# Kernel optimization log

Hardware: AMD Instinct MI355X
Metric: run time of the kernel (lower is better)

## Reference

```python
import jax, jax.numpy as jnp
import numpy as np

B, N, E, P = 8, 4096, 16384, 64   # batch, num_nodes, num_edges, query poses per scene
D, H, MSG, UPD = 256, 512, 256, 254  # node_dim, MLP hidden, msg_sz, update_sz


def setup_inputs() -> dict:
    key = jax.random.key(0)
    ks = jax.random.split(key, 12)
    s = 0.02  # weight scale
    inp = {
        'nodes_states': jax.random.normal(ks[0], (B, N, D), jnp.float32),
        'attn': jax.random.uniform(ks[1], (B, P, N), jnp.float32),
        'W_e1': (jax.random.normal(ks[2], (2 * D, H), jnp.float32) * s),
        'b_e1': jnp.zeros((H,), jnp.float32),
        'W_e2': (jax.random.normal(ks[3], (H, MSG), jnp.float32) * s),
        'b_e2': jnp.zeros((MSG,), jnp.float32),
        'W_n1': (jax.random.normal(ks[4], (D + MSG, H), jnp.float32) * s),
        'b_n1': jnp.zeros((H,), jnp.float32),
        'W_n2': (jax.random.normal(ks[5], (H, UPD), jnp.float32) * s),
        'b_n2': jnp.zeros((UPD,), jnp.float32),
        'edge_sources': jax.random.randint(ks[6], (E,), 0, N, jnp.int32),
        'edge_sinks': jax.random.randint(ks[7], (E,), 0, N, jnp.int32),
        'msg_steps': 3,
    }
    return inp


def reference(nodes_states, attn, W_e1, b_e1, W_e2, b_e2, W_n1, b_n1, W_n2, b_n2,
              edge_sources, edge_sinks, msg_steps):
    ns = nodes_states  # (B, N, D)
    upd_sz = W_n2.shape[-1]
    for _ in range(int(msg_steps)):
        # gather node states along edges
        src = ns[:, edge_sources]            # (B, E, D)
        snk = ns[:, edge_sinks]              # (B, E, D)
        e_in = jnp.concatenate([src, snk], axis=-1)          # (B, E, 2D)
        h = jax.nn.relu(e_in @ W_e1 + b_e1)
        msgs = h @ W_e2 + b_e2                               # (B, E, MSG)
        # scatter-add messages to sink nodes (== torch index_add on dim 1)
        incoming = jnp.zeros((ns.shape[0], ns.shape[1], msgs.shape[-1]), ns.dtype)
        incoming = incoming.at[:, edge_sinks].add(msgs)      # (B, N, MSG)
        # node update MLP
        n_in = jnp.concatenate([incoming, ns], axis=-1)      # (B, N, D+MSG)
        h2 = jax.nn.relu(n_in @ W_n1 + b_n1)
        upd = h2 @ W_n2 + b_n2                               # (B, N, UPD)
        ns = ns.at[:, :, -upd_sz:].add(upd)
    # graph_out_to_out: attention-weighted extraction (torch.bmm)
    extraction = jnp.einsum('bpn,bnd->bpd', attn, ns)        # (B, P, D)
    # num_copies = 0 -> extraction unchanged; unsqueeze(-1).unsqueeze(-1)
    return extraction[..., None, None]
```

## Files before the change

### kernel.cpp

```cpp
#include <hip/hip_runtime.h>
#include <cstddef>
#include <cstdint>

typedef unsigned short u16;
typedef unsigned int u32;
typedef short bf16x8 __attribute__((ext_vector_type(8)));
typedef float f32x4 __attribute__((ext_vector_type(4)));
typedef u32 u32x4 __attribute__((ext_vector_type(4)));

namespace {
constexpr int B_ = 8, N_ = 4096, E_ = 16384, P_ = 64;
constexpr int D_ = 256, H_ = 512, MSG_ = 256, UPD_ = 254;
constexpr int CHUNK_U16 = 16384;
constexpr int NCHUNK = 24;
constexpr float FXS = 16384.0f;
constexpr float FXI = 1.0f / 16384.0f;
}

__device__ inline u16 f2b(float f) {
  u32 u = __float_as_uint(f);
  u += 0x7FFFu + ((u >> 16) & 1u);
  return (u16)(u >> 16);
}
__device__ inline u32 pk2(float a, float b) {
  return (u32)f2b(a) | ((u32)f2b(b) << 16);
}
__device__ inline f32x4 mfma16(bf16x8 a, bf16x8 b, f32x4 c) {
  return __builtin_amdgcn_mfma_f32_16x16x32_bf16(a, b, c, 0, 0, 0);
}
__device__ inline void gload16(const void* g, void* l) {
  __builtin_amdgcn_global_load_lds(
      (const __attribute__((address_space(1))) unsigned int*)g,
      (__attribute__((address_space(3))) unsigned int*)l, 16, 0, 0);
}
__device__ inline void wait_vm8()   { asm volatile("s_waitcnt vmcnt(8)" ::: "memory"); }
__device__ inline void wait_vm0()   { asm volatile("s_waitcnt vmcnt(0)" ::: "memory"); }
__device__ inline void wait_lgkm0() { asm volatile("s_waitcnt lgkmcnt(0)" ::: "memory"); }

__global__ void hist_k(const int* __restrict__ esnk, int* __restrict__ cnt) {
  const int e = blockIdx.x * 256 + threadIdx.x;
  atomicAdd(&cnt[esnk[e]], 1);
}
__global__ __launch_bounds__(256)
void scan_k(const int* __restrict__ cnt, int* __restrict__ rowptr,
            int* __restrict__ cursor) {
  __shared__ int part[257];
  const int t = threadIdx.x;
  int c[16]; int s = 0;
#pragma unroll
  for (int i = 0; i < 16; i++) { c[i] = cnt[t * 16 + i]; s += c[i]; }
  part[t + 1] = s;
  __syncthreads();
  if (t == 0) { part[0] = 0; for (int i = 1; i <= 256; i++) part[i] += part[i - 1]; }
  __syncthreads();
  int off = part[t];
#pragma unroll
  for (int i = 0; i < 16; i++) {
    rowptr[t * 16 + i] = off; cursor[t * 16 + i] = off; off += c[i];
  }
}
__global__ void place_k(const int* __restrict__ esnk, int* __restrict__ cursor,
                        int* __restrict__ order) {
  const int e = blockIdx.x * 256 + threadIdx.x;
  const int p = atomicAdd(&cursor[esnk[e]], 1);
  order[p] = e;
}

__global__ void b16cast_k(const float* __restrict__ src, u16* __restrict__ dst) {
  const int i = blockIdx.x * 256 + threadIdx.x;
  const float4 v0 = ((const float4*)src)[i * 2];
  const float4 v1 = ((const float4*)src)[i * 2 + 1];
  u32x4 pk;
  pk.x = pk2(v0.x, v0.y); pk.y = pk2(v0.z, v0.w);
  pk.z = pk2(v1.x, v1.y); pk.w = pk2(v1.z, v1.w);
  ((u32x4*)dst)[i] = pk;
}

__global__ __launch_bounds__(256, 2)
void edge_mlp(const u16* __restrict__ nsb, u16* __restrict__ msgs,
              const int* __restrict__ esrc, const int* __restrict__ esnk,
              const u16* __restrict__ wpk,
              const float* __restrict__ b1, const float* __restrict__ b2, int g0)
{
  __shared__ alignas(16) u16 Wbuf[2 * CHUNK_U16];

  const int t = threadIdx.x;
  const int w = t >> 6, l = t & 63, r = l & 15, lq = l >> 4;
  const int bl = blockIdx.y, bb = g0 + bl;
  const int e0 = blockIdx.x * 128 + w * 32 + r;
  const int e1 = e0 + 16;

  auto stage = [&](int c, int buf) {
    const u16* gb = wpk + (size_t)c * CHUNK_U16;
    u16* lb = &Wbuf[buf * CHUNK_U16];
#pragma unroll
    for (int s = 0; s < 8; s++) {
      const int sidx = s * 256 + t;
      gload16(gb + (size_t)sidx * 8, lb + sidx * 8);
    }
  };
  stage(0, 0);

  const int nrs0 = esrc[e0], nrk0 = esnk[e0];
  const int nrs1 = esrc[e1], nrk1 = esnk[e1];

  bf16x8 af[2][16];
#pragma unroll
  for (int kt = 0; kt < 16; kt++) {
    const int co = (kt < 8 ? kt : kt - 8) * 32 + lq * 8;
    const int n0 = (kt < 8) ? nrs0 : nrk0;
    const int n1 = (kt < 8) ? nrs1 : nrk1;
    af[0][kt] = *(const bf16x8*)(nsb + ((size_t)bb * N_ + n0) * 256 + co);
    af[1][kt] = *(const bf16x8*)(nsb + ((size_t)bb * N_ + n1) * 256 + co);
  }

  const int s0 = ((2 * lq) & 3) * 16 + r;
  const int s1 = ((2 * lq + 1) & 3) * 16 + r;
  const bool sel = (lq >> 1) != 0;

  auto mk_hB = [&](f32x4 a0, f32x4 a1, float4 bv0, float4 bv1) -> bf16x8 {
    const u32 p00 = pk2(fmaxf(a0[0] + bv0.x, 0.f), fmaxf(a0[1] + bv0.y, 0.f));
    const u32 p01 = pk2(fmaxf(a0[2] + bv0.z, 0.f), fmaxf(a0[3] + bv0.w, 0.f));
    const u32 p10 = pk2(fmaxf(a1[0] + bv1.x, 0.f), fmaxf(a1[1] + bv1.y, 0.f));
    const u32 p11 = pk2(fmaxf(a1[2] + bv1.z, 0.f), fmaxf(a1[3] + bv1.w, 0.f));
    const int t00 = __shfl((int)p00, s0), t10 = __shfl((int)p10, s0);
    const int t01 = __shfl((int)p01, s0), t11 = __shfl((int)p11, s0);
    const int u00 = __shfl((int)p00, s1), u10 = __shfl((int)p10, s1);
    const int u01 = __shfl((int)p01, s1), u11 = __shfl((int)p11, s1);
    u32x4 hb;
    hb.x = (u32)(sel ? t10 : t00); hb.y = (u32)(sel ? t11 : t01);
    hb.z = (u32)(sel ? u10 : u00); hb.w = (u32)(sel ? u11 : u01);
    return __builtin_bit_cast(bf16x8, hb);
  };

  bf16x8 hB[2][16];

#pragma unroll
  for (int P = 0; P < 16; P++) {
    wait_lgkm0();
    __builtin_amdgcn_s_barrier();
    stage(P + 1, (P + 1) & 1);
    wait_vm8();
    __builtin_amdgcn_s_barrier();
    __builtin_amdgcn_sched_barrier(0);
    f32x4 a00 = {}, a01 = {}, a10 = {}, a11 = {};
    const u16* wb = &Wbuf[(P & 1) * CHUNK_U16];
    __builtin_amdgcn_s_setprio(1);
#pragma unroll
    for (int kt = 0; kt < 16; kt++) {
      const bf16x8 w0 = *(const bf16x8*)&wb[((kt * 2 + 0) * 64 + l) * 8];
      const bf16x8 w1 = *(const bf16x8*)&wb[((kt * 2 + 1) * 64 + l) * 8];
      a00 = mfma16(w0, af[0][kt], a00);
      a01 = mfma16(w1, af[0][kt], a01);
      a10 = mfma16(w0, af[1][kt], a10);
      a11 = mfma16(w1, af[1][kt], a11);
    }
    __builtin_amdgcn_s_setprio(0);
    const float4 bv0 = *(const float4*)(b1 + P * 32 + lq * 4);
    const float4 bv1 = *(const float4*)(b1 + P * 32 + 16 + lq * 4);
    hB[0][P] = mk_hB(a00, a01, bv0, bv1);
    hB[1][P] = mk_hB(a10, a11, bv0, bv1);
  }

  u16* mrow0 = msgs + ((size_t)bl * E_ + e0) * 256;
  u16* mrow1 = msgs + ((size_t)bl * E_ + e1) * 256;
#pragma unroll
  for (int Hh = 0; Hh < 2; Hh++) {
    f32x4 acc[4][2][2] = {};
#pragma unroll
    for (int cc = 0; cc < 4; cc++) {
      const int C = Hh * 4 + cc, c = 16 + C;
      wait_lgkm0();
      __builtin_amdgcn_s_barrier();
      if (C < 7) { stage(c + 1, (c + 1) & 1); wait_vm8(); }
      else       { wait_vm0(); }
      __builtin_amdgcn_s_barrier();
      __builtin_amdgcn_sched_barrier(0);
      const u16* wb = &Wbuf[(c & 1) * CHUNK_U16];
      __builtin_amdgcn_s_setprio(1);
#pragma unroll
      for (int kt = 0; kt < 16; kt++) {
        const bf16x8 w0 = *(const bf16x8*)&wb[((kt * 2 + 0) * 64 + l) * 8];
        const bf16x8 w1 = *(const bf16x8*)&wb[((kt * 2 + 1) * 64 + l) * 8];
        acc[cc][0][0] = mfma16(w0, hB[0][kt], acc[cc][0][0]);
        acc[cc][0][1] = mfma16(w1, hB[0][kt], acc[cc][0][1]);
        acc[cc][1][0] = mfma16(w0, hB[1][kt], acc[cc][1][0]);
        acc[cc][1][1] = mfma16(w1, hB[1][kt], acc[cc][1][1]);
      }
      __builtin_amdgcn_s_setprio(0);
    }
#pragma unroll
    for (int cc = 0; cc < 4; cc++) {
      const int C = Hh * 4 + cc;
      const float4 bv0 = *(const float4*)(b2 + C * 32 + lq * 4);
      const float4 bv1 = *(const float4*)(b2 + C * 32 + 16 + lq * 4);
      uint2 q0, q1;
      q0.x = pk2(acc[cc][0][0][0] + bv0.x, acc[cc][0][0][1] + bv0.y);
      q0.y = pk2(acc[cc][0][0][2] + bv0.z, acc[cc][0][0][3] + bv0.w);
      q1.x = pk2(acc[cc][0][1][0] + bv1.x, acc[cc][0][1][1] + bv1.y);
      q1.y = pk2(acc[cc][0][1][2] + bv1.z, acc[cc][0][1][3] + bv1.w);
      *(uint2*)&mrow0[C * 32 + lq * 4]      = q0;
      *(uint2*)&mrow0[C * 32 + 16 + lq * 4] = q1;
      uint2 r0, r1;
      r0.x = pk2(acc[cc][1][0][0] + bv0.x, acc[cc][1][0][1] + bv0.y);
      r0.y = pk2(acc[cc][1][0][2] + bv0.z, acc[cc][1][0][3] + bv0.w);
      r1.x = pk2(acc[cc][1][1][0] + bv1.x, acc[cc][1][1][1] + bv1.y);
      r1.y = pk2(acc[cc][1][1][2] + bv1.z, acc[cc][1][1][3] + bv1.w);
      *(uint2*)&mrow1[C * 32 + lq * 4]      = r0;
      *(uint2*)&mrow1[C * 32 + 16 + lq * 4] = r1;
    }
  }
}

__global__ __launch_bounds__(256)
void gather_k(const u16* __restrict__ msgs, u16* __restrict__ incb,
              const int* __restrict__ order, const int* __restrict__ rowptr,
              const int* __restrict__ cnt, int g0)
{
  const int t = threadIdx.x;
  const int n = blockIdx.x * 4 + (t >> 6);
  const int l = t & 63;
  const int bl = blockIdx.y, bb = g0 + bl;
  const int c0 = l * 4;
  int sA = 0, sB = 0, sC = 0, sD = 0;
  const int beg = rowptr[n], num = cnt[n];
  for (int i = 0; i < num; i++) {
    const int e = order[beg + i];
    const uint2 p = *(const uint2*)(msgs + ((size_t)bl * E_ + e) * 256 + c0);
    sA += __float2int_rn(__uint_as_float(p.x << 16) * FXS);
    sB += __float2int_rn(__uint_as_float(p.x & 0xFFFF0000u) * FXS);
    sC += __float2int_rn(__uint_as_float(p.y << 16) * FXS);
    sD += __float2int_rn(__uint_as_float(p.y & 0xFFFF0000u) * FXS);
  }
  uint2 o;
  o.x = pk2((float)sA * FXI, (float)sB * FXI);
  o.y = pk2((float)sC * FXI, (float)sD * FXI);
  *(uint2*)(incb + ((size_t)bb * N_ + n) * 256 + c0) = o;
}

__global__ __launch_bounds__(256, 1)
void node_mlp(float* __restrict__ ns, u16* __restrict__ nsb,
              const u16* __restrict__ incb, const u16* __restrict__ wpk,
              const float* __restrict__ b1, const float* __restrict__ b2)
{
  __shared__ alignas(16) u16 Wbuf[2 * CHUNK_U16];

  const int t = threadIdx.x;
  const int w = t >> 6, l = t & 63, r = l & 15, lq = l >> 4;
  const int bb = blockIdx.y;
  const int row0 = blockIdx.x * 128 + w * 32 + r;
  const int row1 = row0 + 16;

  auto stage = [&](int c, int buf) {
    const u16* gb = wpk + (size_t)c * CHUNK_U16;
    u16* lb = &Wbuf[buf * CHUNK_U16];
#pragma unroll
    for (int s = 0; s < 8; s++) {
      const int sidx = s * 256 + t;
      gload16(gb + (size_t)sidx * 8, lb + sidx * 8);
    }
  };
  stage(0, 0);

  bf16x8 af[2][16];
#pragma unroll
  for (int kt = 0; kt < 16; kt++) {
    if (kt < 8) {
      af[0][kt] = *(const bf16x8*)(incb + ((size_t)bb * N_ + row0) * 256 + kt * 32 + lq * 8);
      af[1][kt] = *(const bf16x8*)(incb + ((size_t)bb * N_ + row1) * 256 + kt * 32 + lq * 8);
    } else {
      const int co = (kt - 8) * 32 + lq * 8;
      af[0][kt] = *(const bf16x8*)(nsb + ((size_t)bb * N_ + row0) * 256 + co);
      af[1][kt] = *(const bf16x8*)(nsb + ((size_t)bb * N_ + row1) * 256 + co);
    }
  }

  const int s0 = ((2 * lq) & 3) * 16 + r;
  const int s1 = ((2 * lq + 1) & 3) * 16 + r;
  const bool sel = (lq >> 1) != 0;

  auto mk_hB = [&](f32x4 a0, f32x4 a1, float4 bv0, float4 bv1) -> bf16x8 {
    const u32 p00 = pk2(fmaxf(a0[0] + bv0.x, 0.f), fmaxf(a0[1] + bv0.y, 0.f));
    const u32 p01 = pk2(fmaxf(a0[2] + bv0.z, 0.f), fmaxf(a0[3] + bv0.w, 0.f));
    const u32 p10 = pk2(fmaxf(a1[0] + bv1.x, 0.f), fmaxf(a1[1] + bv1.y, 0.f));
    const u32 p11 = pk2(fmaxf(a1[2] + bv1.z, 0.f), fmaxf(a1[3] + bv1.w, 0.f));
    const int t00 = __shfl((int)p00, s0), t10 = __shfl((int)p10, s0);
    const int t01 = __shfl((int)p01, s0), t11 = __shfl((int)p11, s0);
    const int u00 = __shfl((int)p00, s1), u10 = __shfl((int)p10, s1);
    const int u01 = __shfl((int)p01, s1), u11 = __shfl((int)p11, s1);
    u32x4 hb;
    hb.x = (u32)(sel ? t10 : t00); hb.y = (u32)(sel ? t11 : t01);
    hb.z = (u32)(sel ? u10 : u00); hb.w = (u32)(sel ? u11 : u01);
    return __builtin_bit_cast(bf16x8, hb);
  };

  bf16x8 hB[2][16];

#pragma unroll
  for (int P = 0; P < 16; P++) {
    wait_lgkm0();
    __builtin_amdgcn_s_barrier();
    stage(P + 1, (P + 1) & 1);
    wait_vm8();
    __builtin_amdgcn_s_barrier();
    __builtin_amdgcn_sched_barrier(0);
    f32x4 a00 = {}, a01 = {}, a10 = {}, a11 = {};
    const u16* wb = &Wbuf[(P & 1) * CHUNK_U16];
    __builtin_amdgcn_s_setprio(1);
#pragma unroll
    for (int kt = 0; kt < 16; kt++) {
      const bf16x8 w0 = *(const bf16x8*)&wb[((kt * 2 + 0) * 64 + l) * 8];
      const bf16x8 w1 = *(const bf16x8*)&wb[((kt * 2 + 1) * 64 + l) * 8];
      a00 = mfma16(w0, af[0][kt], a00);
      a01 = mfma16(w1, af[0][kt], a01);
      a10 = mfma16(w0, af[1][kt], a10);
      a11 = mfma16(w1, af[1][kt], a11);
    }
    __builtin_amdgcn_s_setprio(0);
    const float4 bv0 = *(const float4*)(b1 + P * 32 + lq * 4);
    const float4 bv1 = *(const float4*)(b1 + P * 32 + 16 + lq * 4);
    hB[0][P] = mk_hB(a00, a01, bv0, bv1);
    hB[1][P] = mk_hB(a10, a11, bv0, bv1);
  }

  float* nsrow0 = ns + ((size_t)bb * N_ + row0) * 256;
  float* nsrow1 = ns + ((size_t)bb * N_ + row1) * 256;
  u16* mbrow0 = nsb + ((size_t)bb * N_ + row0) * 256;
  u16* mbrow1 = nsb + ((size_t)bb * N_ + row1) * 256;
#pragma unroll
  for (int Hh = 0; Hh < 2; Hh++) {
    f32x4 acc[4][2][2] = {};
#pragma unroll
    for (int cc = 0; cc < 4; cc++) {
      const int C = Hh * 4 + cc, c = 16 + C;
      wait_lgkm0();
      __builtin_amdgcn_s_barrier();
      if (C < 7) { stage(c + 1, (c + 1) & 1); wait_vm8(); }
      else       { wait_vm0(); }
      __builtin_amdgcn_s_barrier();
      __builtin_amdgcn_sched_barrier(0);
      const u16* wb = &Wbuf[(c & 1) * CHUNK_U16];
      __builtin_amdgcn_s_setprio(1);
#pragma unroll
      for (int kt = 0; kt < 16; kt++) {
        const bf16x8 w0 = *(const bf16x8*)&wb[((kt * 2 + 0) * 64 + l) * 8];
        const bf16x8 w1 = *(const bf16x8*)&wb[((kt * 2 + 1) * 64 + l) * 8];
        acc[cc][0][0] = mfma16(w0, hB[0][kt], acc[cc][0][0]);
        acc[cc][0][1] = mfma16(w1, hB[0][kt], acc[cc][0][1]);
        acc[cc][1][0] = mfma16(w0, hB[1][kt], acc[cc][1][0]);
        acc[cc][1][1] = mfma16(w1, hB[1][kt], acc[cc][1][1]);
      }
      __builtin_amdgcn_s_setprio(0);
    }
#pragma unroll
    for (int cc = 0; cc < 4; cc++) {
      const int C = Hh * 4 + cc;
      const float4 bv0 = *(const float4*)(b2 + C * 32 + lq * 4);
      const float4 bv1 = *(const float4*)(b2 + C * 32 + 16 + lq * 4);
      const int uA = C * 32 + lq * 4, uB = uA + 16;
#pragma unroll
      for (int g = 0; g < 2; g++) {
        float* nsrow = g ? nsrow1 : nsrow0;
        u16* mrow = g ? mbrow1 : mbrow0;
        const f32x4 a0 = acc[cc][g][0], a1 = acc[cc][g][1];
        float2* pA = (float2*)(nsrow + 2 + uA);
        float2 v0 = pA[0]; v0.x += a0[0] + bv0.x; v0.y += a0[1] + bv0.y; pA[0] = v0;
        float2 v1 = pA[1]; v1.x += a0[2] + bv0.z; v1.y += a0[3] + bv0.w; pA[1] = v1;
        *(u32*)(mrow + 2 + uA)     = pk2(v0.x, v0.y);
        *(u32*)(mrow + 2 + uA + 2) = pk2(v1.x, v1.y);
        float2* pB = (float2*)(nsrow + 2 + uB);
        float2 u0 = pB[0]; u0.x += a1[0] + bv1.x; u0.y += a1[1] + bv1.y; pB[0] = u0;
        *(u32*)(mrow + 2 + uB) = pk2(u0.x, u0.y);
        if (uB + 3 < UPD_) {
          float2 u1 = pB[1]; u1.x += a1[2] + bv1.z; u1.y += a1[3] + bv1.w; pB[1] = u1;
          *(u32*)(mrow + 2 + uB + 2) = pk2(u1.x, u1.y);
        }
      }
    }
  }
}

__global__ void pack_w(const float* __restrict__ W1, const float* __restrict__ W2,
                       int ldw2, int nv2, u16* __restrict__ out)
{
  const int idx = blockIdx.x * 256 + threadIdx.x;
  const int c = idx >> 11, s = idx & 2047;
  const int kt = s >> 7, i01 = (s >> 6) & 1, l = s & 63;
  const int r = l & 15, lq = l >> 4;
  const int kbase = kt * 32 + lq * 8;
  const int colt = i01 * 16 + r;
  u16 v[8];
  if (c < 16) {
    const int col = c * 32 + colt;
#pragma unroll
    for (int i = 0; i < 8; i++) v[i] = f2b(W1[(size_t)(kbase + i) * 512 + col]);
  } else {
    const int n2 = (c - 16) * 32 + colt;
#pragma unroll
    for (int i = 0; i < 8; i++)
      v[i] = (n2 < nv2) ? f2b(W2[(size_t)(kbase + i) * ldw2 + n2]) : (u16)0;
  }
  u32x4 pk;
  pk.x = (u32)v[0] | ((u32)v[1] << 16);
  pk.y = (u32)v[2] | ((u32)v[3] << 16);
  pk.z = (u32)v[4] | ((u32)v[5] << 16);
  pk.w = (u32)v[6] | ((u32)v[7] << 16);
  *(u32x4*)(out + (size_t)idx * 8) = pk;
}

__global__ __launch_bounds__(256)
void extract_k(const float* __restrict__ attn, const float* __restrict__ nsb,
               float* __restrict__ out)
{
  __shared__ float a_s[16][64];
  const int b = blockIdx.x, pc = blockIdx.y, kc = blockIdx.z;
  const int d = threadIdx.x;
  float acc[16] = {};
  const int nbase0 = kc * 128;

  for (int nb = 0; nb < 128; nb += 64) {
    const int nbase = nbase0 + nb;
    __syncthreads();
#pragma unroll
    for (int lp = 0; lp < 4; lp++) {
      const int idx = lp * 256 + threadIdx.x;
      const int pi = idx >> 6, j = idx & 63;
      a_s[pi][j] = attn[((size_t)b * P_ + pc * 16 + pi) * N_ + nbase + j];
    }
    __syncthreads();
#pragma unroll 8
    for (int j = 0; j < 64; j++) {
      const float v = nsb[((size_t)b * N_ + nbase + j) * D_ + d];
#pragma unroll
      for (int i = 0; i < 16; i++) acc[i] += a_s[i][j] * v;
    }
  }
#pragma unroll
  for (int i = 0; i < 16; i++)
    atomicAdd(&out[((size_t)b * P_ + pc * 16 + i) * D_ + d], acc[i]);
}

extern "C" void kernel_launch(void* const* d_in, const int* in_sizes, int n_in,
                              void* d_out, int out_size, void* d_ws, size_t ws_size,
                              hipStream_t stream)
{
  const float* nodes = (const float*)d_in[0];
  const float* attn  = (const float*)d_in[1];
  const float* W_e1  = (const float*)d_in[2];
  const float* b_e1  = (const float*)d_in[3];
  const float* W_e2  = (const float*)d_in[4];
  const float* b_e2  = (const float*)d_in[5];
  const float* W_n1  = (const float*)d_in[6];
  const float* b_n1  = (const float*)d_in[7];
  const float* W_n2  = (const float*)d_in[8];
  const float* b_n2  = (const float*)d_in[9];
  const int* esrc    = (const int*)d_in[10];
  const int* esnk    = (const int*)d_in[11];

  float* ns   = (float*)d_ws;
  u16* incb   = (u16*)(ns + (size_t)B_ * N_ * D_);
  u16* nsb16  = incb + (size_t)B_ * N_ * MSG_;
  u16* msgs   = nsb16 + (size_t)B_ * N_ * D_;

  const size_t fixed_b = (size_t)B_ * N_ * D_ * 4 + (size_t)B_ * N_ * MSG_ * 2
                       + (size_t)B_ * N_ * D_ * 2
                       + (size_t)2 * NCHUNK * CHUNK_U16 * 2 + (size_t)16 * N_ + 4096;
  const int gb = (ws_size >= fixed_b + (size_t)4 * E_ * MSG_ * 2) ? 4 : 2;

  u16* wpkE   = msgs + (size_t)gb * E_ * MSG_;
  u16* wpkN   = wpkE + (size_t)NCHUNK * CHUNK_U16;
  int* cnt    = (int*)(wpkN + (size_t)NCHUNK * CHUNK_U16);
  int* rowptr = cnt + N_;
  int* cursor = rowptr + N_;
  int* order  = cursor + N_;
  float* out  = (float*)d_out;

  hipMemcpyAsync(ns, nodes, sizeof(float) * (size_t)B_ * N_ * D_,
                 hipMemcpyDeviceToDevice, stream);
  b16cast_k<<<dim3(B_ * N_ * D_ / 8 / 256), dim3(256), 0, stream>>>(nodes, nsb16);
  pack_w<<<dim3(192), dim3(256), 0, stream>>>(W_e1, W_e2, MSG_, MSG_, wpkE);
  pack_w<<<dim3(192), dim3(256), 0, stream>>>(W_n1, W_n2, UPD_, UPD_, wpkN);

  hipMemsetAsync(cnt, 0, sizeof(int) * N_, stream);
  hist_k<<<dim3(E_ / 256), dim3(256), 0, stream>>>(esnk, cnt);
  scan_k<<<dim3(1), dim3(256), 0, stream>>>(cnt, rowptr, cursor);
  place_k<<<dim3(E_ / 256), dim3(256), 0, stream>>>(esnk, cursor, order);

  for (int s = 0; s < 3; s++) {
    for (int g0 = 0; g0 < B_; g0 += gb) {
      edge_mlp<<<dim3(E_ / 128, gb), dim3(256), 0, stream>>>(
          nsb16, msgs, esrc, esnk, wpkE, b_e1, b_e2, g0);
      gather_k<<<dim3(N_ / 4, gb), dim3(256), 0, stream>>>(
          msgs, incb, order, rowptr, cnt, g0);
    }
    node_mlp<<<dim3(N_ / 128, B_), dim3(256), 0, stream>>>(
        ns, nsb16, incb, wpkN, b_n1, b_n2);
  }

  hipMemsetAsync(out, 0, sizeof(float) * (size_t)out_size, stream);
  extract_k<<<dim3(B_, P_ / 16, 32), dim3(256), 0, stream>>>(attn, ns, out);
}
```

Baseline: 800.1 us.

## Interleave weight-chunk prefetch with MFMA loop and use single barrier per chunk

Weight chunk staging into LDS moves from a block of eight global-to-LDS loads before each chunk into the MFMA inner loop, one load per kt iteration. The two barriers and the vmcnt(8) wait per chunk become a single boundary after the chunk's compute that waits for all loads and LDS reads. The aim is to overlap the weight fetch with matrix work and cut barrier overhead, in both the edge and node MLP kernels. The trade-off is a full vmcnt(0) wait at every chunk, so any load latency not hidden by the compute is exposed directly.

```diff
diff --git a/kernel.cpp b/kernel.cpp
--- a/kernel.cpp
+++ b/kernel.cpp
@@ -33,9 +33,14 @@
       (const __attribute__((address_space(1))) unsigned int*)g,
       (__attribute__((address_space(3))) unsigned int*)l, 16, 0, 0);
 }
-__device__ inline void wait_vm8()   { asm volatile("s_waitcnt vmcnt(8)" ::: "memory"); }
 __device__ inline void wait_vm0()   { asm volatile("s_waitcnt vmcnt(0)" ::: "memory"); }
 __device__ inline void wait_lgkm0() { asm volatile("s_waitcnt lgkmcnt(0)" ::: "memory"); }
+__device__ inline void chunk_boundary() {
+  wait_lgkm0();
+  wait_vm0();
+  __builtin_amdgcn_s_barrier();
+  __builtin_amdgcn_sched_barrier(0);
+}
 
 __global__ void hist_k(const int* __restrict__ esnk, int* __restrict__ cnt) {
   const int e = blockIdx.x * 256 + threadIdx.x;
@@ -90,16 +95,14 @@
   const int e0 = blockIdx.x * 128 + w * 32 + r;
   const int e1 = e0 + 16;
 
-  auto stage = [&](int c, int buf) {
+  auto stage1 = [&](int c, int s) {
     const u16* gb = wpk + (size_t)c * CHUNK_U16;
-    u16* lb = &Wbuf[buf * CHUNK_U16];
-#pragma unroll
-    for (int s = 0; s < 8; s++) {
-      const int sidx = s * 256 + t;
-      gload16(gb + (size_t)sidx * 8, lb + sidx * 8);
-    }
+    u16* lb = &Wbuf[(c & 1) * CHUNK_U16];
+    const int sidx = s * 256 + t;
+    gload16(gb + (size_t)sidx * 8, lb + sidx * 8);
   };
-  stage(0, 0);
+#pragma unroll
+  for (int s = 0; s < 8; s++) stage1(0, s);
 
   const int nrs0 = esrc[e0], nrk0 = esnk[e0];
   const int nrs1 = esrc[e1], nrk1 = esnk[e1];
@@ -113,6 +116,7 @@
     af[0][kt] = *(const bf16x8*)(nsb + ((size_t)bb * N_ + n0) * 256 + co);
     af[1][kt] = *(const bf16x8*)(nsb + ((size_t)bb * N_ + n1) * 256 + co);
   }
+  chunk_boundary();
 
   const int s0 = ((2 * lq) & 3) * 16 + r;
   const int s1 = ((2 * lq + 1) & 3) * 16 + r;
@@ -137,17 +141,12 @@
 
 #pragma unroll
   for (int P = 0; P < 16; P++) {
-    wait_lgkm0();
-    __builtin_amdgcn_s_barrier();
-    stage(P + 1, (P + 1) & 1);
-    wait_vm8();
-    __builtin_amdgcn_s_barrier();
-    __builtin_amdgcn_sched_barrier(0);
     f32x4 a00 = {}, a01 = {}, a10 = {}, a11 = {};
     const u16* wb = &Wbuf[(P & 1) * CHUNK_U16];
     __builtin_amdgcn_s_setprio(1);
 #pragma unroll
     for (int kt = 0; kt < 16; kt++) {
+      if (kt < 8) stage1(P + 1, kt);
       const bf16x8 w0 = *(const bf16x8*)&wb[((kt * 2 + 0) * 64 + l) * 8];
       const bf16x8 w1 = *(const bf16x8*)&wb[((kt * 2 + 1) * 64 + l) * 8];
       a00 = mfma16(w0, af[0][kt], a00);
@@ -160,6 +159,7 @@
     const float4 bv1 = *(const float4*)(b1 + P * 32 + 16 + lq * 4);
     hB[0][P] = mk_hB(a00, a01, bv0, bv1);
     hB[1][P] = mk_hB(a10, a11, bv0, bv1);
+    chunk_boundary();
   }
 
   u16* mrow0 = msgs + ((size_t)bl * E_ + e0) * 256;
@@ -170,16 +170,11 @@
 #pragma unroll
     for (int cc = 0; cc < 4; cc++) {
       const int C = Hh * 4 + cc, c = 16 + C;
-      wait_lgkm0();
-      __builtin_amdgcn_s_barrier();
-      if (C < 7) { stage(c + 1, (c + 1) & 1); wait_vm8(); }
-      else       { wait_vm0(); }
-      __builtin_amdgcn_s_barrier();
-      __builtin_amdgcn_sched_barrier(0);
       const u16* wb = &Wbuf[(c & 1) * CHUNK_U16];
       __builtin_amdgcn_s_setprio(1);
 #pragma unroll
       for (int kt = 0; kt < 16; kt++) {
+        if (kt < 8 && C < 7) stage1(c + 1, kt);
         const bf16x8 w0 = *(const bf16x8*)&wb[((kt * 2 + 0) * 64 + l) * 8];
         const bf16x8 w1 = *(const bf16x8*)&wb[((kt * 2 + 1) * 64 + l) * 8];
         acc[cc][0][0] = mfma16(w0, hB[0][kt], acc[cc][0][0]);
@@ -188,6 +183,7 @@
         acc[cc][1][1] = mfma16(w1, hB[1][kt], acc[cc][1][1]);
       }
       __builtin_amdgcn_s_setprio(0);
+      if (C < 7) chunk_boundary();
     }
 #pragma unroll
     for (int cc = 0; cc < 4; cc++) {
@@ -251,16 +247,14 @@
   const int row0 = blockIdx.x * 128 + w * 32 + r;
   const int row1 = row0 + 16;
 
-  auto stage = [&](int c, int buf) {
+  auto stage1 = [&](int c, int s) {
     const u16* gb = wpk + (size_t)c * CHUNK_U16;
-    u16* lb = &Wbuf[buf * CHUNK_U16];
-#pragma unroll
-    for (int s = 0; s < 8; s++) {
-      const int sidx = s * 256 + t;
-      gload16(gb + (size_t)sidx * 8, lb + sidx * 8);
-    }
+    u16* lb = &Wbuf[(c & 1) * CHUNK_U16];
+    const int sidx = s * 256 + t;
+    gload16(gb + (size_t)sidx * 8, lb + sidx * 8);
   };
-  stage(0, 0);
+#pragma unroll
+  for (int s = 0; s < 8; s++) stage1(0, s);
 
   bf16x8 af[2][16];
 #pragma unroll
@@ -274,6 +268,7 @@
       af[1][kt] = *(const bf16x8*)(nsb + ((size_t)bb * N_ + row1) * 256 + co);
     }
   }
+  chunk_boundary();
 
   const int s0 = ((2 * lq) & 3) * 16 + r;
   const int s1 = ((2 * lq + 1) & 3) * 16 + r;
@@ -298,17 +293,12 @@
 
 #pragma unroll
   for (int P = 0; P < 16; P++) {
-    wait_lgkm0();
-    __builtin_amdgcn_s_barrier();
-    stage(P + 1, (P + 1) & 1);
-    wait_vm8();
-    __builtin_amdgcn_s_barrier();
-    __builtin_amdgcn_sched_barrier(0);
     f32x4 a00 = {}, a01 = {}, a10 = {}, a11 = {};
     const u16* wb = &Wbuf[(P & 1) * CHUNK_U16];
     __builtin_amdgcn_s_setprio(1);
 #pragma unroll
     for (int kt = 0; kt < 16; kt++) {
+      if (kt < 8) stage1(P + 1, kt);
       const bf16x8 w0 = *(const bf16x8*)&wb[((kt * 2 + 0) * 64 + l) * 8];
       const bf16x8 w1 = *(const bf16x8*)&wb[((kt * 2 + 1) * 64 + l) * 8];
       a00 = mfma16(w0, af[0][kt], a00);
@@ -321,6 +311,7 @@
     const float4 bv1 = *(const float4*)(b1 + P * 32 + 16 + lq * 4);
     hB[0][P] = mk_hB(a00, a01, bv0, bv1);
     hB[1][P] = mk_hB(a10, a11, bv0, bv1);
+    chunk_boundary();
   }
 
   float* nsrow0 = ns + ((size_t)bb * N_ + row0) * 256;
@@ -333,16 +324,11 @@
 #pragma unroll
     for (int cc = 0; cc < 4; cc++) {
       const int C = Hh * 4 + cc, c = 16 + C;
-      wait_lgkm0();
-      __builtin_amdgcn_s_barrier();
-      if (C < 7) { stage(c + 1, (c + 1) & 1); wait_vm8(); }
-      else       { wait_vm0(); }
-      __builtin_amdgcn_s_barrier();
-      __builtin_amdgcn_sched_barrier(0);
       const u16* wb = &Wbuf[(c & 1) * CHUNK_U16];
       __builtin_amdgcn_s_setprio(1);
 #pragma unroll
       for (int kt = 0; kt < 16; kt++) {
+        if (kt < 8 && C < 7) stage1(c + 1, kt);
         const bf16x8 w0 = *(const bf16x8*)&wb[((kt * 2 + 0) * 64 + l) * 8];
         const bf16x8 w1 = *(const bf16x8*)&wb[((kt * 2 + 1) * 64 + l) * 8];
         acc[cc][0][0] = mfma16(w0, hB[0][kt], acc[cc][0][0]);
@@ -351,6 +337,7 @@
         acc[cc][1][1] = mfma16(w1, hB[1][kt], acc[cc][1][1]);
       }
       __builtin_amdgcn_s_setprio(0);
+      if (C < 7) chunk_boundary();
     }
 #pragma unroll
     for (int cc = 0; cc < 4; cc++) {
```

Result: faster. 779.0 us (-2.6%).
